# Performance work log

Hardware: AMD Instinct MI355X
Metric: run time of the kernel (lower is better)

## Reference

```python
import math
import jax, jax.numpy as jnp
import numpy as np

NUM_CLASSES = 80
CONF_THR = 0.05
IOU_THR = 0.5
MAX_PER_CLASS = 100
MAX_DET = 100
PRE_NMS_K = 200  # per-class candidates kept before greedy NMS (>= max_per_class)
BOX_VAR = np.array([0.1, 0.1, 0.2, 0.2], np.float32)
IMG_H, IMG_W = 640, 640
BATCH = 8


def _anchor_dims():
    ratios = [0.5, 1.0, 2.0]
    scales = [2.0 ** x for x in (0.0, 1.0 / 3.0, 2.0 / 3.0)]
    dims_all = []
    for area in [32.0 ** 2, 64.0 ** 2, 128.0 ** 2, 256.0 ** 2, 512.0 ** 2]:
        dims = []
        for r in ratios:  # ratio-major, scale-minor (matches AnchorBox._compute_dims)
            h = math.sqrt(area / r)
            w = area / h
            for s in scales:
                dims.append([s * w, s * h])
        dims_all.append(np.array(dims, np.float32))  # [9, 2]
    return dims_all


def get_anchors(H, W):
    """Anchors in [cx, cy, w, h], shape [total_anchors, 4] (static, numpy)."""
    strides = [8, 16, 32, 64, 128]
    out = []
    for stride, dims in zip(strides, _anchor_dims()):
        fh, fw = math.ceil(H / stride), math.ceil(W / stride)
        rx = (np.arange(fw, dtype=np.float32) + 0.5) * stride
        ry = (np.arange(fh, dtype=np.float32) + 0.5) * stride
        cx, cy = np.meshgrid(rx, ry)  # each [fh, fw], 'xy' indexing like tf.meshgrid
        centers = np.broadcast_to(np.stack([cx, cy], -1)[:, :, None, :], (fh, fw, 9, 2))
        d = np.broadcast_to(dims[None, None], (fh, fw, 9, 2))
        out.append(np.concatenate([centers, d], -1).reshape(-1, 4))
    return jnp.asarray(np.concatenate(out, 0))


def decode_boxes(anchors, box_pred):
    """Apply variance scaling + anchor offsets, return corner boxes."""
    b = box_pred * jnp.asarray(BOX_VAR)
    xy = b[..., :2] * anchors[..., 2:] + anchors[..., :2]
    wh = jnp.exp(b[..., 2:]) * anchors[..., 2:]
    return jnp.concatenate([xy - wh * 0.5, xy + wh * 0.5], axis=-1)


def pairwise_iou(b):
    lt = jnp.maximum(b[:, None, :2], b[None, :, :2])
    rb = jnp.minimum(b[:, None, 2:], b[None, :, 2:])
    wh = jnp.maximum(rb - lt, 0.0)
    inter = wh[..., 0] * wh[..., 1]
    area = (b[:, 2] - b[:, 0]) * (b[:, 3] - b[:, 1])
    return inter / (area[:, None] + area[None, :] - inter + 1e-8)


def nms_one_class(boxes, scores):
    """Greedy NMS over top PRE_NMS_K candidates for one class."""
    sc, idx = jax.lax.top_k(scores, PRE_NMS_K)
    bb = boxes[idx]  # [K, 4]
    valid = sc > CONF_THR
    iou = jax.lax.stop_gradient(pairwise_iou(bb))  # [K, K]
    ar = jnp.arange(PRE_NMS_K)

    def body(i, keep):
        supp = keep[i] & (iou[i] > IOU_THR) & (ar > i)
        return keep & ~supp

    keep = jax.lax.fori_loop(0, PRE_NMS_K, body, valid)
    sc = jnp.where(keep, sc, 0.0)
    sc2, j = jax.lax.top_k(sc, MAX_PER_CLASS)
    bb2 = jnp.where((sc2 > 0.0)[:, None], bb[j], 0.0)
    return bb2, sc2


def detect_one_image(boxes, cls_scores):
    """boxes [A,4] shared across classes, cls_scores [A,C]."""
    cb, cs = jax.vmap(nms_one_class, in_axes=(None, 1))(boxes, cls_scores)  # [C,100,4],[C,100]
    cls_id = jnp.broadcast_to(
        jnp.arange(NUM_CLASSES, dtype=jnp.float32)[:, None], cs.shape
    )
    flat_s = cs.reshape(-1)
    flat_b = cb.reshape(-1, 4)
    flat_c = cls_id.reshape(-1)
    s, i = jax.lax.top_k(flat_s, MAX_DET)
    b = jnp.where((s > 0.0)[:, None], flat_b[i], 0.0)
    c = jnp.where(s > 0.0, flat_c[i], 0.0)
    n = jnp.sum(s > 0.0).astype(jnp.int32)
    return b, s, c, n


def setup_inputs() -> dict:
    key = jax.random.key(0)
    k1, _ = jax.random.split(key)
    images = jnp.zeros((BATCH, IMG_H, IMG_W, 3), jnp.float32)  # only shape is used
    num_anchors = 76725  # 640x640 image -> (6400+1600+400+100+25)*9
    predictions = jax.random.normal(k1, (BATCH, num_anchors, 4 + NUM_CLASSES), jnp.float32)
    return {"images": images, "predictions": predictions}


def reference(images, predictions):
    H, W = images.shape[1], images.shape[2]
    anchors = get_anchors(H, W)  # [A, 4]
    box_pred = predictions[:, :, :4]
    cls_pred = jax.nn.sigmoid(predictions[:, :, 4:])  # [B, A, C]
    boxes = decode_boxes(anchors[None], box_pred)  # [B, A, 4]
    nmsed_boxes, nmsed_scores, nmsed_classes, valid = jax.vmap(detect_one_image)(
        boxes, cls_pred
    )
    return nmsed_boxes, nmsed_scores, nmsed_classes, valid
```

## Files before the change

### kernel.cpp

```cpp
#include <hip/hip_runtime.h>
#include <stdint.h>

typedef unsigned long long u64;
typedef unsigned int u32;
typedef unsigned char u8;

#define NB 8
#define NA 76725
#define NC 80
#define NCH 84
#define PRE_K 200
#define MAXPC 100
#define MAXDET 100
#define F4_PER_IMG (NA * 21u)

#define T0 0.93f
#define XCUT 2.58f
#define BLKX 256
#define SPAN (BLKX * 256u)
#define NSTEP 24
#define LCAP 24
#define CAP2 512
#define CAPF 2048


__device__ __forceinline__ float sigmoid_ref(float x) {
    return 1.0f / (1.0f + expf(-x));
}

__device__ void decode_box(float4 d, int a, float4* box, float* areaOut) {
    int lvl, off, fw, stride;
    if (a < 57600)      { lvl = 0; off = 0;     fw = 80; stride = 8;   }
    else if (a < 72000) { lvl = 1; off = 57600; fw = 40; stride = 16;  }
    else if (a < 75600) { lvl = 2; off = 72000; fw = 20; stride = 32;  }
    else if (a < 76500) { lvl = 3; off = 75600; fw = 10; stride = 64;  }
    else                { lvl = 4; off = 76500; fw = 5;  stride = 128; }
    int idx  = a - off;
    int k    = idx % 9;
    int cell = idx / 9;
    int row = cell / fw, col = cell - row * fw;
    float cx = __fmul_rn((float)col + 0.5f, (float)stride);
    float cy = __fmul_rn((float)row + 0.5f, (float)stride);
    int ri = k / 3, si = k - ri * 3;
    double r    = (ri == 0) ? 0.5 : ((ri == 1) ? 1.0 : 2.0);
    double side = (double)(32 << lvl);
    double area = side * side;
    double h = sqrt(area / r);
    double w = area / h;
    double s = exp2((double)si / 3.0);
    float aw = (float)(s * w);
    float ah = (float)(s * h);
    float b0 = __fmul_rn(d.x, 0.1f);
    float b1 = __fmul_rn(d.y, 0.1f);
    float b2 = __fmul_rn(d.z, 0.2f);
    float b3 = __fmul_rn(d.w, 0.2f);
    float ux = __fadd_rn(__fmul_rn(b0, aw), cx);
    float uy = __fadd_rn(__fmul_rn(b1, ah), cy);
    float wx = __fmul_rn(expf(b2), aw);
    float wy = __fmul_rn(expf(b3), ah);
    float hx = __fmul_rn(wx, 0.5f);
    float hy = __fmul_rn(wy, 0.5f);
    float x1 = __fsub_rn(ux, hx), y1 = __fsub_rn(uy, hy);
    float x2 = __fadd_rn(ux, hx), y2 = __fadd_rn(uy, hy);
    *box = make_float4(x1, y1, x2, y2);
    *areaOut = __fmul_rn(__fsub_rn(x2, x1), __fsub_rn(y2, y1));
}


__device__ __forceinline__ void scan4(float4 v, u32 idx,
                                      u32* lhist, u64 (*llist)[LCAP]) {
    u32 a  = idx / 21u;
    u32 c4 = idx - a * 21u;
    if (c4 == 0u) return;
    float m = fmaxf(fmaxf(v.x, v.y), fmaxf(v.z, v.w));
    if (m <= XCUT) return;
    u32 cb = c4 * 4u - 4u;
    float vv[4] = {v.x, v.y, v.z, v.w};
#pragma unroll
    for (int q = 0; q < 4; ++q) {
        if (vv[q] > XCUT) {
            float sig = sigmoid_ref(vv[q]);
            if (sig > T0) {
                u32 c = cb + (u32)q;
                u64 key = ((u64)__float_as_uint(sig) << 32) | (u64)(~a);
                u32 p = atomicAdd(&lhist[c], 1u);
                if (p < LCAP) llist[c][p] = key;
            }
        }
    }
}

__global__ __launch_bounds__(256, 8) void k_scan(const float4* __restrict__ p4,
                                                 u64* __restrict__ seg,
                                                 u32* __restrict__ cntT) {
    __shared__ u32 lhist[NC];
    __shared__ u64 llist[NC][LCAP];
    u32 b = blockIdx.y, x = blockIdx.x;
    for (u32 c = threadIdx.x; c < NC; c += 256u) lhist[c] = 0u;
    __syncthreads();

    const float4* base = p4 + (u64)b * F4_PER_IMG;
    u32 i0 = x * 256u + threadIdx.x;
#pragma unroll 1
    for (int s = 0; s < NSTEP; s += 8) {
        u32 ia = i0 + (u32)s * SPAN;
        float4 v[8];
#pragma unroll
        for (int q = 0; q < 8; ++q) v[q] = base[ia + (u32)q * SPAN];
#pragma unroll
        for (int q = 0; q < 8; ++q)
            scan4(v[q], ia + (u32)q * SPAN, lhist, llist);
    }
    {
        u32 it = i0 + (u32)NSTEP * SPAN;
        if (it < F4_PER_IMG) scan4(base[it], it, lhist, llist);
    }
    __syncthreads();

    if (threadIdx.x < NC) {
        u32 c = threadIdx.x;
        u32 n = lhist[c];
        u32 m = n < LCAP ? n : (u32)LCAP;
        u64* o = seg + ((u64)(b * NC + c) * BLKX + x) * LCAP;
        for (u32 j = 0; j < m; ++j) o[j] = llist[c][j];
        cntT[(b * NC + c) * BLKX + x] = n;
    }
}


__global__ __launch_bounds__(512) void k_nms(const float* __restrict__ pred,
                                             const u64* __restrict__ seg,
                                             const u32* __restrict__ cntT,
                                             float* __restrict__ sc2,
                                             float* __restrict__ bb2) {
    int bc = blockIdx.x;
    int b = bc / NC, c = bc % NC;
    __shared__ u64 keys[CAP2];
    __shared__ u64 sorted[PRE_K];
    __shared__ u32 wsum[4];
    __shared__ u32 oflow[4];
    __shared__ u32 mc[BLKX];
    __shared__ u32 ex[BLKX];
    __shared__ float4 box[PRE_K];
    __shared__ u32 rsupA[PRE_K][8];
    __shared__ u32 validw[8];
    __shared__ u32 keepw[8];
    __shared__ u64 red[512];

    u32 tid = threadIdx.x, lane = tid & 63u, wv = tid >> 6;

    u32 m_c = 0, incv = 0;
    if (tid < 256u) {
        u32 n_raw = cntT[(u64)bc * BLKX + tid];
        m_c = n_raw < LCAP ? n_raw : (u32)LCAP;
        mc[tid] = m_c;
        u32 v = m_c;
#pragma unroll
        for (u32 d = 1; d < 64u; d <<= 1) {
            u32 t = __shfl_up(v, d, 64);
            if (lane >= d) v += t;
        }
        u64 ob = __ballot(n_raw > (u32)LCAP);
        if (lane == 63u) wsum[wv] = v;
        if (lane == 0u)  oflow[wv] = (ob != 0ull) ? 1u : 0u;
        incv = v;
    }
    __syncthreads();
    if (tid < 256u) {
        u32 off = 0;
        for (u32 w = 0; w < wv; ++w) off += wsum[w];
        ex[tid] = incv + off - m_c;
    }
    u32 total = wsum[0] + wsum[1] + wsum[2] + wsum[3];
    bool over = (oflow[0] | oflow[1] | oflow[2] | oflow[3]) != 0u;
    bool repaired = over || (total < (u32)PRE_K) || (total > (u32)CAP2);
    __syncthreads();

    if (!repaired) {
        const u64* segrow = seg + (u64)bc * (BLKX * LCAP);
        for (u32 i = tid; i < (u32)(BLKX * LCAP); i += 512u) {
            u32 x = i / (u32)LCAP;
            u32 j = i - x * (u32)LCAP;
            if (j < mc[x]) keys[ex[x] + j] = segrow[i];
        }
        for (u32 i = tid; i < (u32)CAP2; i += 512u)
            if (i >= total) keys[i] = 0ull;
        __syncthreads();
        u64 ka = (tid < total) ? keys[tid] : 0ull;
        u32 ra = 0, j = 0;
        for (; j + 8u <= total; j += 8u) {
            u64 c0 = keys[j],     c1 = keys[j + 1], c2 = keys[j + 2], c3 = keys[j + 3];
            u64 c4 = keys[j + 4], c5 = keys[j + 5], c6 = keys[j + 6], c7 = keys[j + 7];
            ra += ((c0 > ka) ? 1u : 0u) + ((c1 > ka) ? 1u : 0u)
                + ((c2 > ka) ? 1u : 0u) + ((c3 > ka) ? 1u : 0u)
                + ((c4 > ka) ? 1u : 0u) + ((c5 > ka) ? 1u : 0u)
                + ((c6 > ka) ? 1u : 0u) + ((c7 > ka) ? 1u : 0u);
        }
        for (; j < total; ++j) ra += (keys[j] > ka) ? 1u : 0u;
        if (tid < total && ra < (u32)PRE_K) sorted[ra] = ka;
        __syncthreads();
    } else {
        u64 cur = ~0ull;
        for (int k = 0; k < PRE_K; ++k) {
            u64 loc = 0;
            for (int a = tid; a < NA; a += 512) {
                float xx = pred[((long)b * NA + a) * NCH + 4 + c];
                float sg = sigmoid_ref(xx);
                u64 key  = ((u64)__float_as_uint(sg) << 32) | (u64)(~(u32)a);
                if (key < cur && key > loc) loc = key;
            }
            red[tid] = loc;
            __syncthreads();
            for (int s = 256; s > 0; s >>= 1) {
                if (tid < (u32)s) {
                    if (red[tid + s] > red[tid]) red[tid] = red[tid + s];
                }
                __syncthreads();
            }
            cur = red[0];
            if (tid == 0) sorted[k] = cur;
            __syncthreads();
        }
    }

    for (u32 i = tid; i < (u32)PRE_K * 8u; i += 512u) rsupA[i >> 3][i & 7u] = 0u;
    if (tid < 8u) validw[tid] = 0u;
    __syncthreads();

    bool val = false;
    float4 mybox = make_float4(0.f, 0.f, 0.f, 0.f);
    if (tid < (u32)PRE_K) {
        u64 key = sorted[tid];
        float sig = __uint_as_float((u32)(key >> 32));
        int a = (int)(~(u32)key);
        if (sig > 0.05f) {
            float4 dd = *(const float4*)(pred + ((long)b * NA + a) * NCH);
            float ar;
            decode_box(dd, a, &mybox, &ar);
            val = true;
        }
        box[tid] = mybox;
    }
    u64 vbal = __ballot(val);
    if (lane == 0u && wv < 4u) {
        validw[2u * wv]      = (u32)vbal;
        validw[2u * wv + 1u] = (u32)(vbal >> 32);
    }
    __syncthreads();

    for (u32 p = tid; p < (u32)(PRE_K * PRE_K); p += 512u) {
        u32 i  = p / (u32)PRE_K;
        u32 jx = p - i * (u32)PRE_K;
        if (jx > i) {
            float4 bi = box[i], bj = box[jx];
            float ai = __fmul_rn(__fsub_rn(bi.z, bi.x), __fsub_rn(bi.w, bi.y));
            float aj = __fmul_rn(__fsub_rn(bj.z, bj.x), __fsub_rn(bj.w, bj.y));
            float ltx = fmaxf(bi.x, bj.x), lty = fmaxf(bi.y, bj.y);
            float rbx = fminf(bi.z, bj.z), rby = fminf(bi.w, bj.w);
            float wx = fmaxf(__fsub_rn(rbx, ltx), 0.f);
            float wy = fmaxf(__fsub_rn(rby, lty), 0.f);
            float inter = __fmul_rn(wx, wy);
            float den = __fadd_rn(__fsub_rn(__fadd_rn(ai, aj), inter), 1e-8f);
            float iou = __fdiv_rn(inter, den);
            if (iou > 0.5f) atomicOr(&rsupA[jx][i >> 5], 1u << (i & 31u));
        }
    }
    __syncthreads();

    if (tid < 64u) {
        u32 l = tid;
        uint4 sA0 = *(const uint4*)&rsupA[l][0];
        uint4 sA1 = *(const uint4*)&rsupA[l][4];
        uint4 sB0 = *(const uint4*)&rsupA[l + 64u][0];
        uint4 sB1 = *(const uint4*)&rsupA[l + 64u][4];
        uint4 sC0 = *(const uint4*)&rsupA[l + 128u][0];
        uint4 sC1 = *(const uint4*)&rsupA[l + 128u][4];
        uint4 sD0 = make_uint4(0u, 0u, 0u, 0u);
        uint4 sD1 = make_uint4(0u, 0u, 0u, 0u);
        if (l < 8u) {
            sD0 = *(const uint4*)&rsupA[l + 192u][0];
            sD1 = *(const uint4*)&rsupA[l + 192u][4];
        }
        u32 v0 = validw[0], v1 = validw[1], v2 = validw[2], v3 = validw[3];
        u32 v4 = validw[4], v5 = validw[5], v6 = validw[6];
        u32 vb0 = (u32)(((((u64)v1 << 32) | v0) >> l) & 1ull);
        u32 vb1 = (u32)(((((u64)v3 << 32) | v2) >> l) & 1ull);
        u32 vb2 = (u32)(((((u64)v5 << 32) | v4) >> l) & 1ull);
        u32 vb3 = (l < 8u) ? ((v6 >> l) & 1u) : 0u;
        u32 k0 = v0, k1 = v1, k2 = v2, k3 = v3, k4 = v4, k5 = v5, k6 = v6;
        for (int t = 0; t < PRE_K; ++t) {
            u32 s0 = (k0 & sA0.x) | (k1 & sA0.y) | (k2 & sA0.z) | (k3 & sA0.w)
                   | (k4 & sA1.x) | (k5 & sA1.y) | (k6 & sA1.z);
            u32 s1 = (k0 & sB0.x) | (k1 & sB0.y) | (k2 & sB0.z) | (k3 & sB0.w)
                   | (k4 & sB1.x) | (k5 & sB1.y) | (k6 & sB1.z);
            u32 s2 = (k0 & sC0.x) | (k1 & sC0.y) | (k2 & sC0.z) | (k3 & sC0.w)
                   | (k4 & sC1.x) | (k5 & sC1.y) | (k6 & sC1.z);
            u32 s3 = (k0 & sD0.x) | (k1 & sD0.y) | (k2 & sD0.z) | (k3 & sD0.w)
                   | (k4 & sD1.x) | (k5 & sD1.y) | (k6 & sD1.z);
            bool n0 = vb0 && (s0 == 0u);
            bool n1 = vb1 && (s1 == 0u);
            bool n2 = vb2 && (s2 == 0u);
            bool n3 = (vb3 != 0u) && (s3 == 0u);
            u64 B0 = __ballot(n0), B1 = __ballot(n1), B2 = __ballot(n2), B3 = __ballot(n3);
            u32 nk0 = (u32)B0, nk1 = (u32)(B0 >> 32);
            u32 nk2 = (u32)B1, nk3 = (u32)(B1 >> 32);
            u32 nk4 = (u32)B2, nk5 = (u32)(B2 >> 32);
            u32 nk6 = (u32)B3;
            bool same = (nk0 == k0) && (nk1 == k1) && (nk2 == k2) && (nk3 == k3)
                     && (nk4 == k4) && (nk5 == k5) && (nk6 == k6);
            k0 = nk0; k1 = nk1; k2 = nk2; k3 = nk3; k4 = nk4; k5 = nk5; k6 = nk6;
            if (same) break;
        }
        if (l == 0u) {
            keepw[0] = k0; keepw[1] = k1; keepw[2] = k2; keepw[3] = k3;
            keepw[4] = k4; keepw[5] = k5; keepw[6] = k6;
        }
    }
    __syncthreads();

    int kept = 0;
#pragma unroll
    for (int w = 0; w < 7; ++w) kept += __popc(keepw[w]);
    if (kept > MAXPC) kept = MAXPC;

    if (tid >= (u32)kept && tid < (u32)MAXPC) {
        int pos = tid;
        sc2[bc * MAXPC + pos] = 0.f;
        float* o = bb2 + ((long)bc * MAXPC + pos) * 4;
        o[0] = 0.f; o[1] = 0.f; o[2] = 0.f; o[3] = 0.f;
    }
    if (tid < (u32)PRE_K) {
        int r = tid;
        if ((keepw[r >> 5] >> (r & 31)) & 1u) {
            int pos = 0;
            for (int w = 0; w < (r >> 5); ++w) pos += __popc(keepw[w]);
            pos += __popc(keepw[r >> 5] & ((1u << (r & 31)) - 1u));
            if (pos < MAXPC) {
                u64 key = sorted[r];
                float sig = __uint_as_float((u32)(key >> 32));
                sc2[bc * MAXPC + pos] = sig;
                float* o = bb2 + ((long)bc * MAXPC + pos) * 4;
                o[0] = mybox.x; o[1] = mybox.y; o[2] = mybox.z; o[3] = mybox.w;
            }
        }
    }
}


__global__ __launch_bounds__(1024) void k_final(const float* __restrict__ sc2,
                                                const float* __restrict__ bb2,
                                                float* __restrict__ out) {
    int b = blockIdx.x;
    __shared__ u32 hist[256];
    __shared__ u32 sfx[256];
    __shared__ u64 keys[CAPF];
    __shared__ u64 top[128];
    __shared__ u32 cnt_s;
    __shared__ int t_s;
    __shared__ u64 red[1024];

    for (int i = threadIdx.x; i < 256; i += blockDim.x) hist[i] = 0u;
    if (threadIdx.x < 128) top[threadIdx.x] = 0ull;
    if (threadIdx.x == 0) { cnt_s = 0u; t_s = 0; }
    __syncthreads();

    const float* s_b = sc2 + b * (NC * MAXPC);
    for (int f = threadIdx.x; f < NC * MAXPC; f += blockDim.x) {
        float s = s_b[f];
        if (s > 0.f) {
            int bin = (int)(s * 256.f); if (bin > 255) bin = 255;
            atomicAdd(&hist[bin], 1u);
        }
    }
    __syncthreads();

    if (threadIdx.x < 256) sfx[threadIdx.x] = hist[threadIdx.x];
    __syncthreads();
    for (u32 d = 1; d < 256u; d <<= 1) {
        u32 v = 0;
        if (threadIdx.x < 256u && threadIdx.x + d < 256u) v = sfx[threadIdx.x + d];
        __syncthreads();
        if (threadIdx.x < 256u) sfx[threadIdx.x] += v;
        __syncthreads();
    }
    if (threadIdx.x < 256) {
        bool ge = sfx[threadIdx.x] >= (u32)MAXDET;
        bool nlt = (threadIdx.x == 255) || (sfx[threadIdx.x + 1] < (u32)MAXDET);
        if (ge && nlt) t_s = (int)threadIdx.x;
    }
    __syncthreads();
    int t = t_s;

    for (int f = threadIdx.x; f < NC * MAXPC; f += blockDim.x) {
        float s = s_b[f];
        if (s > 0.f) {
            int bin = (int)(s * 256.f); if (bin > 255) bin = 255;
            if (bin >= t) {
                u32 pos = atomicAdd(&cnt_s, 1u);
                if (pos < CAPF)
                    keys[pos] = ((u64)__float_as_uint(s) << 32) | (u64)(~(u32)f);
            }
        }
    }
    __syncthreads();
    u32 g = cnt_s;

    if (g <= (u32)CAPF) {
        u64 ka = (threadIdx.x < g) ? keys[threadIdx.x] : 0ull;
        u64 kb = (threadIdx.x + 1024u < g) ? keys[threadIdx.x + 1024u] : 0ull;
        u32 ra = 0, rb = 0, j = 0;
        for (; j + 8u <= g; j += 8u) {
            u64 c0 = keys[j],     c1 = keys[j + 1], c2 = keys[j + 2], c3 = keys[j + 3];
            u64 c4 = keys[j + 4], c5 = keys[j + 5], c6 = keys[j + 6], c7 = keys[j + 7];
            ra += ((c0 > ka) ? 1u : 0u) + ((c1 > ka) ? 1u : 0u)
                + ((c2 > ka) ? 1u : 0u) + ((c3 > ka) ? 1u : 0u)
                + ((c4 > ka) ? 1u : 0u) + ((c5 > ka) ? 1u : 0u)
                + ((c6 > ka) ? 1u : 0u) + ((c7 > ka) ? 1u : 0u);
            rb += ((c0 > kb) ? 1u : 0u) + ((c1 > kb) ? 1u : 0u)
                + ((c2 > kb) ? 1u : 0u) + ((c3 > kb) ? 1u : 0u)
                + ((c4 > kb) ? 1u : 0u) + ((c5 > kb) ? 1u : 0u)
                + ((c6 > kb) ? 1u : 0u) + ((c7 > kb) ? 1u : 0u);
        }
        for (; j < g; ++j) {
            u64 kj = keys[j];
            ra += (kj > ka) ? 1u : 0u;
            rb += (kj > kb) ? 1u : 0u;
        }
        if (threadIdx.x < g && ra < (u32)MAXDET) top[ra] = ka;
        if (threadIdx.x + 1024u < g && rb < (u32)MAXDET) top[rb] = kb;
        __syncthreads();
    } else {
        u64 cur = ~0ull;
        for (int k = 0; k < MAXDET; ++k) {
            u64 loc = 0;
            for (int f = threadIdx.x; f < NC * MAXPC; f += blockDim.x) {
                float s = s_b[f];
                if (s > 0.f) {
                    u64 key = ((u64)__float_as_uint(s) << 32) | (u64)(~(u32)f);
                    if (key < cur && key > loc) loc = key;
                }
            }
            red[threadIdx.x] = loc;
            __syncthreads();
            for (int st = 512; st > 0; st >>= 1) {
                if (threadIdx.x < (u32)st) {
                    if (red[threadIdx.x + st] > red[threadIdx.x])
                        red[threadIdx.x] = red[threadIdx.x + st];
                }
                __syncthreads();
            }
            cur = red[0];
            if (threadIdx.x == 0) top[k] = cur;
            __syncthreads();
        }
        if (threadIdx.x == 0) {
            u32 nv = 0;
            for (int r = 0; r < MAXDET; ++r) if (top[r] != 0ull) ++nv;
            cnt_s = nv;
        }
        __syncthreads();
        g = cnt_s;
    }

    if (threadIdx.x < MAXDET) {
        int r = threadIdx.x;
        u64 key = top[r];
        u32 hi = (u32)(key >> 32);
        float s = 0.f, cf = 0.f;
        float bx0 = 0.f, bx1 = 0.f, bx2 = 0.f, bx3 = 0.f;
        if (hi != 0u) {
            s = __uint_as_float(hi);
            int f = (int)(~(u32)key);
            int c = f / MAXPC, jj = f - c * MAXPC;
            const float* bsrc = bb2 + ((long)(b * NC + c) * MAXPC + jj) * 4;
            bx0 = bsrc[0]; bx1 = bsrc[1]; bx2 = bsrc[2]; bx3 = bsrc[3];
            cf = (float)c;
        }
        float* ob = out + ((long)b * MAXDET + r) * 4;
        ob[0] = bx0; ob[1] = bx1; ob[2] = bx2; ob[3] = bx3;
        out[NB * MAXDET * 4 + b * MAXDET + r] = s;
        out[NB * MAXDET * 4 + NB * MAXDET + b * MAXDET + r] = cf;
    }
    if (threadIdx.x == 0) {
        u32 nv = g < (u32)MAXDET ? g : (u32)MAXDET;
        out[NB * MAXDET * 4 + 2 * NB * MAXDET + b] = (float)nv;
    }
}


extern "C" void kernel_launch(void* const* d_in, const int* in_sizes, int n_in,
                              void* d_out, int out_size, void* d_ws, size_t ws_size,
                              hipStream_t stream) {
    const float* pred = (const float*)d_in[1];
    if (n_in >= 2 && in_sizes[0] == NB * NA * NCH) pred = (const float*)d_in[0];

    char* ws = (char*)d_ws;
    const long BCN = (long)NB * NC;
    u64* seg   = (u64*)ws;
    char* p    = ws + BCN * BLKX * LCAP * 8;
    u32* cntT  = (u32*)p;            p += BCN * BLKX * 4;
    float* sc2 = (float*)p;          p += BCN * MAXPC * 4;
    float* bb2 = (float*)p;

    k_scan <<<dim3(BLKX, NB), 256, 0, stream>>>((const float4*)pred, seg, cntT);
    k_nms  <<<dim3(NB * NC),  512, 0, stream>>>(pred, seg, cntT, sc2, bb2);
    k_final<<<dim3(NB),      1024, 0, stream>>>(sc2, bb2, (float*)d_out);
}
```

Measured before the change: 107.2 us.

## Split candidate scan into per-anchor bitmask pass and sparse extraction pass

```diff
diff --git a/kernel.cpp b/kernel.cpp
--- a/kernel.cpp
+++ b/kernel.cpp
@@ -12,13 +12,10 @@
 #define PRE_K 200
 #define MAXPC 100
 #define MAXDET 100
-#define F4_PER_IMG (NA * 21u)
 
 #define T0 0.93f
 #define XCUT 2.58f
 #define BLKX 256
-#define SPAN (BLKX * 256u)
-#define NSTEP 24
 #define LCAP 24
 #define CAP2 512
 #define CAPF 2048
@@ -67,62 +64,70 @@
 }
 
 
-__device__ __forceinline__ void scan4(float4 v, u32 idx,
-                                      u32* lhist, u64 (*llist)[LCAP]) {
-    u32 a  = idx / 21u;
-    u32 c4 = idx - a * 21u;
-    if (c4 == 0u) return;
-    float m = fmaxf(fmaxf(v.x, v.y), fmaxf(v.z, v.w));
-    if (m <= XCUT) return;
-    u32 cb = c4 * 4u - 4u;
-    float vv[4] = {v.x, v.y, v.z, v.w};
+__global__ __launch_bounds__(256, 4) void k_mask(const float* __restrict__ pred,
+                                                 u32* __restrict__ mask) {
+    u32 b = blockIdx.y;
+    const float* base = pred + (u64)b * NA * NCH;
+    for (u32 a = blockIdx.x * 256u + threadIdx.x; a < (u32)NA; a += (u32)(BLKX * 256)) {
+        const float4* ap = (const float4*)(base + (u64)a * NCH);
+        u32 m = 0;
 #pragma unroll
-    for (int q = 0; q < 4; ++q) {
-        if (vv[q] > XCUT) {
-            float sig = sigmoid_ref(vv[q]);
-            if (sig > T0) {
-                u32 c = cb + (u32)q;
-                u64 key = ((u64)__float_as_uint(sig) << 32) | (u64)(~a);
-                u32 p = atomicAdd(&lhist[c], 1u);
-                if (p < LCAP) llist[c][p] = key;
-            }
-        }
-    }
-}
-
-__global__ __launch_bounds__(256, 8) void k_scan(const float4* __restrict__ p4,
-                                                 u64* __restrict__ seg,
-                                                 u32* __restrict__ cntT) {
+        for (int g = 0; g < 10; ++g) {
+            float4 v = ap[g + 1];
+            float mx = fmaxf(fmaxf(v.x, v.y), fmaxf(v.z, v.w));
+            m |= (mx > XCUT) ? (1u << g) : 0u;
+        }
+#pragma unroll
+        for (int g = 10; g < 20; ++g) {
+            float4 v = ap[g + 1];
+            float mx = fmaxf(fmaxf(v.x, v.y), fmaxf(v.z, v.w));
+            m |= (mx > XCUT) ? (1u << g) : 0u;
+        }
+        mask[(u64)b * NA + a] = m;
+    }
+}
+
+
+__global__ __launch_bounds__(256, 4) void k_extract(const float* __restrict__ pred,
+                                                    const u32* __restrict__ mask,
+                                                    u64* __restrict__ seg,
+                                                    u32* __restrict__ cntT) {
     __shared__ u32 lhist[NC];
     __shared__ u64 llist[NC][LCAP];
     u32 b = blockIdx.y, x = blockIdx.x;
     for (u32 c = threadIdx.x; c < NC; c += 256u) lhist[c] = 0u;
     __syncthreads();
 
-    const float4* base = p4 + (u64)b * F4_PER_IMG;
-    u32 i0 = x * 256u + threadIdx.x;
-#pragma unroll 1
-    for (int s = 0; s < NSTEP; s += 8) {
-        u32 ia = i0 + (u32)s * SPAN;
-        float4 v[8];
+    const float* base = pred + (u64)b * NA * NCH;
+    for (u32 a = x * 256u + threadIdx.x; a < (u32)NA; a += (u32)(BLKX * 256)) {
+        u32 m = mask[(u64)b * NA + a];
+        while (m) {
+            u32 g = (u32)__ffs(m) - 1u;
+            m &= m - 1u;
+            float4 v = *((const float4*)(base + (u64)a * NCH) + 1 + g);
+            float vv[4] = {v.x, v.y, v.z, v.w};
 #pragma unroll
-        for (int q = 0; q < 8; ++q) v[q] = base[ia + (u32)q * SPAN];
-#pragma unroll
-        for (int q = 0; q < 8; ++q)
-            scan4(v[q], ia + (u32)q * SPAN, lhist, llist);
-    }
-    {
-        u32 it = i0 + (u32)NSTEP * SPAN;
-        if (it < F4_PER_IMG) scan4(base[it], it, lhist, llist);
+            for (int q = 0; q < 4; ++q) {
+                if (vv[q] > XCUT) {
+                    float sig = sigmoid_ref(vv[q]);
+                    if (sig > T0) {
+                        u32 c = g * 4u + (u32)q;
+                        u64 key = ((u64)__float_as_uint(sig) << 32) | (u64)(~a);
+                        u32 p = atomicAdd(&lhist[c], 1u);
+                        if (p < LCAP) llist[c][p] = key;
+                    }
+                }
+            }
+        }
     }
     __syncthreads();
 
     if (threadIdx.x < NC) {
         u32 c = threadIdx.x;
         u32 n = lhist[c];
-        u32 m = n < LCAP ? n : (u32)LCAP;
+        u32 mm = n < LCAP ? n : (u32)LCAP;
         u64* o = seg + ((u64)(b * NC + c) * BLKX + x) * LCAP;
-        for (u32 j = 0; j < m; ++j) o[j] = llist[c][j];
+        for (u32 j = 0; j < mm; ++j) o[j] = llist[c][j];
         cntT[(b * NC + c) * BLKX + x] = n;
     }
 }
@@ -500,9 +505,11 @@
     char* p    = ws + BCN * BLKX * LCAP * 8;
     u32* cntT  = (u32*)p;            p += BCN * BLKX * 4;
     float* sc2 = (float*)p;          p += BCN * MAXPC * 4;
-    float* bb2 = (float*)p;
-
-    k_scan <<<dim3(BLKX, NB), 256, 0, stream>>>((const float4*)pred, seg, cntT);
-    k_nms  <<<dim3(NB * NC),  512, 0, stream>>>(pred, seg, cntT, sc2, bb2);
-    k_final<<<dim3(NB),      1024, 0, stream>>>(sc2, bb2, (float*)d_out);
-}
+    float* bb2 = (float*)p;          p += BCN * MAXPC * 16;
+    u32* mask  = (u32*)p;
+
+    k_mask   <<<dim3(BLKX, NB), 256, 0, stream>>>(pred, mask);
+    k_extract<<<dim3(BLKX, NB), 256, 0, stream>>>(pred, mask, seg, cntT);
+    k_nms    <<<dim3(NB * NC),  512, 0, stream>>>(pred, seg, cntT, sc2, bb2);
+    k_final  <<<dim3(NB),      1024, 0, stream>>>(sc2, bb2, (float*)d_out);
+}
```

Measured after the change: 148.3 us. 1.38x slower.

## Split scan into ballot bitmask pass and sparse extraction pass

Applied to the files above, without the earlier changes.

```diff
diff --git a/kernel.cpp b/kernel.cpp
--- a/kernel.cpp
+++ b/kernel.cpp
@@ -12,7 +12,8 @@
 #define PRE_K 200
 #define MAXPC 100
 #define MAXDET 100
-#define F4_PER_IMG (NA * 21u)
+#define F4 1611225u
+#define NW 25176u
 
 #define T0 0.93f
 #define XCUT 2.58f
@@ -67,40 +68,13 @@
 }
 
 
-__device__ __forceinline__ void scan4(float4 v, u32 idx,
-                                      u32* lhist, u64 (*llist)[LCAP]) {
-    u32 a  = idx / 21u;
-    u32 c4 = idx - a * 21u;
-    if (c4 == 0u) return;
-    float m = fmaxf(fmaxf(v.x, v.y), fmaxf(v.z, v.w));
-    if (m <= XCUT) return;
-    u32 cb = c4 * 4u - 4u;
-    float vv[4] = {v.x, v.y, v.z, v.w};
-#pragma unroll
-    for (int q = 0; q < 4; ++q) {
-        if (vv[q] > XCUT) {
-            float sig = sigmoid_ref(vv[q]);
-            if (sig > T0) {
-                u32 c = cb + (u32)q;
-                u64 key = ((u64)__float_as_uint(sig) << 32) | (u64)(~a);
-                u32 p = atomicAdd(&lhist[c], 1u);
-                if (p < LCAP) llist[c][p] = key;
-            }
-        }
-    }
-}
-
-__global__ __launch_bounds__(256, 8) void k_scan(const float4* __restrict__ p4,
-                                                 u64* __restrict__ seg,
-                                                 u32* __restrict__ cntT) {
-    __shared__ u32 lhist[NC];
-    __shared__ u64 llist[NC][LCAP];
-    u32 b = blockIdx.y, x = blockIdx.x;
-    for (u32 c = threadIdx.x; c < NC; c += 256u) lhist[c] = 0u;
-    __syncthreads();
-
-    const float4* base = p4 + (u64)b * F4_PER_IMG;
-    u32 i0 = x * 256u + threadIdx.x;
+__global__ __launch_bounds__(256, 8) void k_mask(const float4* __restrict__ p4,
+                                                 u64* __restrict__ mask) {
+    u32 b = blockIdx.y;
+    u32 lane = threadIdx.x & 63u;
+    const float4* base = p4 + (u64)b * F4;
+    u64* mrow = mask + (u64)b * NW;
+    u32 i0 = blockIdx.x * 256u + threadIdx.x;
 #pragma unroll 1
     for (int s = 0; s < NSTEP; s += 8) {
         u32 ia = i0 + (u32)s * SPAN;
@@ -108,21 +82,72 @@
 #pragma unroll
         for (int q = 0; q < 8; ++q) v[q] = base[ia + (u32)q * SPAN];
 #pragma unroll
-        for (int q = 0; q < 8; ++q)
-            scan4(v[q], ia + (u32)q * SPAN, lhist, llist);
+        for (int q = 0; q < 8; ++q) {
+            float4 t = v[q];
+            bool bit = fmaxf(fmaxf(t.x, t.y), fmaxf(t.z, t.w)) > XCUT;
+            u64 bal = __ballot(bit);
+            if (lane == 0u) mrow[(ia + (u32)q * SPAN) >> 6] = bal;
+        }
     }
     {
         u32 it = i0 + (u32)NSTEP * SPAN;
-        if (it < F4_PER_IMG) scan4(base[it], it, lhist, llist);
+        bool bit = false;
+        if (it < F4) {
+            float4 t = base[it];
+            bit = fmaxf(fmaxf(t.x, t.y), fmaxf(t.z, t.w)) > XCUT;
+        }
+        u64 bal = __ballot(bit);
+        if (lane == 0u && it < F4) mrow[it >> 6] = bal;
+    }
+}
+
+
+__global__ __launch_bounds__(256, 4) void k_extract(const float4* __restrict__ p4,
+                                                    const u64* __restrict__ mask,
+                                                    u64* __restrict__ seg,
+                                                    u32* __restrict__ cntT) {
+    __shared__ u32 lhist[NC];
+    __shared__ u64 llist[NC][LCAP];
+    u32 b = blockIdx.y, x = blockIdx.x;
+    for (u32 c = threadIdx.x; c < NC; c += 256u) lhist[c] = 0u;
+    __syncthreads();
+
+    const float4* base = p4 + (u64)b * F4;
+    u32 w = x * 256u + threadIdx.x;
+    if (w < NW) {
+        u64 m = mask[(u64)b * NW + w];
+        while (m) {
+            u32 bit = (u32)__ffsll((long long)m) - 1u;
+            m &= m - 1ull;
+            u32 idx = w * 64u + bit;
+            u32 a   = idx / 21u;
+            u32 c4  = idx - a * 21u;
+            if (c4 == 0u) continue;
+            float4 v = base[idx];
+            u32 cb = c4 * 4u - 4u;
+            float vv[4] = {v.x, v.y, v.z, v.w};
+#pragma unroll
+            for (int q = 0; q < 4; ++q) {
+                if (vv[q] > XCUT) {
+                    float sig = sigmoid_ref(vv[q]);
+                    if (sig > T0) {
+                        u32 c = cb + (u32)q;
+                        u64 key = ((u64)__float_as_uint(sig) << 32) | (u64)(~a);
+                        u32 p = atomicAdd(&lhist[c], 1u);
+                        if (p < LCAP) llist[c][p] = key;
+                    }
+                }
+            }
+        }
     }
     __syncthreads();
 
     if (threadIdx.x < NC) {
         u32 c = threadIdx.x;
         u32 n = lhist[c];
-        u32 m = n < LCAP ? n : (u32)LCAP;
+        u32 mm = n < LCAP ? n : (u32)LCAP;
         u64* o = seg + ((u64)(b * NC + c) * BLKX + x) * LCAP;
-        for (u32 j = 0; j < m; ++j) o[j] = llist[c][j];
+        for (u32 j = 0; j < mm; ++j) o[j] = llist[c][j];
         cntT[(b * NC + c) * BLKX + x] = n;
     }
 }
@@ -500,9 +525,11 @@
     char* p    = ws + BCN * BLKX * LCAP * 8;
     u32* cntT  = (u32*)p;            p += BCN * BLKX * 4;
     float* sc2 = (float*)p;          p += BCN * MAXPC * 4;
-    float* bb2 = (float*)p;
-
-    k_scan <<<dim3(BLKX, NB), 256, 0, stream>>>((const float4*)pred, seg, cntT);
-    k_nms  <<<dim3(NB * NC),  512, 0, stream>>>(pred, seg, cntT, sc2, bb2);
-    k_final<<<dim3(NB),      1024, 0, stream>>>(sc2, bb2, (float*)d_out);
-}
+    float* bb2 = (float*)p;          p += BCN * MAXPC * 16;
+    u64* mask  = (u64*)p;
+
+    k_mask   <<<dim3(BLKX, NB), 256, 0, stream>>>((const float4*)pred, mask);
+    k_extract<<<dim3(BLKX, NB), 256, 0, stream>>>((const float4*)pred, mask, seg, cntT);
+    k_nms    <<<dim3(NB * NC),  512, 0, stream>>>(pred, seg, cntT, sc2, bb2);
+    k_final  <<<dim3(NB),      1024, 0, stream>>>(sc2, bb2, (float*)d_out);
+}
```

Result: slower. 112.0 us (+4.4%).
